# Performance work log

Measured on AMD Instinct MI355X. Metric: run time of the kernel, lower is better.

Reference implementation:

```python
import math
import jax, jax.numpy as jnp
from jax import lax
import numpy as np

HIDDEN = 128
KQ_CH = HIDDEN * 3  # 384
H, W = 48, 64
N = 4


def _conv(x, w, pad, dil):
    # NCHW conv, OIHW weights, stride 1
    return lax.conv_general_dilated(
        x, w, window_strides=(1, 1),
        padding=[(pad, pad), (pad, pad)],
        rhs_dilation=(dil, dil),
        dimension_numbers=("NCHW", "OIHW", "NCHW"))


def _lrelu(x):
    return jnp.where(x >= 0, x, 0.2 * x)


def setup_inputs() -> dict:
    key = jax.random.key(0)
    ks = jax.random.split(key, 7)
    s = 0.05
    return {
        "k": jax.random.normal(ks[0], (N, KQ_CH, H, W), jnp.float32),
        "q": jax.random.normal(ks[1], (N, KQ_CH, H, W), jnp.float32),
        "v": jax.random.normal(ks[2], (N, HIDDEN, H, W), jnp.float32),
        "w_value": jax.random.normal(ks[3], (HIDDEN, HIDDEN, 1, 1), jnp.float32) * s,
        "w_out": jax.random.normal(ks[4], (HIDDEN, HIDDEN, 3, 3), jnp.float32) * s,
        "w_ff1": jax.random.normal(ks[5], (HIDDEN, HIDDEN, 3, 3), jnp.float32) * s,
        "w_ff2": jax.random.normal(ks[6], (HIDDEN, HIDDEN, 3, 3), jnp.float32) * s,
    }


def reference(k, q, v, w_value, w_out, w_ff1, w_ff2):
    n, c, h, w = k.shape  # c = kq_channels
    hw = h * w
    # value embedding: 1x1 conv
    val = _conv(v, w_value, 0, 1)  # [n, hidden, h, w]
    kf = k.reshape(n, c, hw)
    qf = q.reshape(n, c, hw)
    # scores[n, key_pos, query_pos] = k^T q / sqrt(c)
    scores = jnp.einsum("nck,ncq->nkq", kf, qf) / math.sqrt(c)
    # softmax over key positions (torch dim=-2)
    p_attn = jax.nn.softmax(scores, axis=1)  # [n, hw, hw]
    # p_val = value @ p_attn
    p_val = jnp.einsum("ndk,nkq->ndq", val.reshape(n, -1, hw), p_attn)
    p_val = p_val.reshape(v.shape)
    # residual update with output_linear (conv3x3 + LeakyReLU)
    v2 = v + _lrelu(_conv(p_val, w_out, 1, 1))
    # dilated-conv feed forward with residual
    ff = _lrelu(_conv(_lrelu(_conv(v2, w_ff1, 2, 2)), w_ff2, 1, 1))
    return v2 + ff
```

## Files before the change

kernel.cpp:

```cpp
#include <hip/hip_runtime.h>

#define NB  4
#define CKQ 384
#define DH  128
#define HH  48
#define WW  64
#define HW  3072

#define NSPLIT 16
#define KSEG  (HW / NSPLIT)
#define BQ 128
#define BK 32
#define VSP 40
#define PTS 40

typedef short bf16x8 __attribute__((ext_vector_type(8)));
typedef short b16x4  __attribute__((ext_vector_type(4)));
typedef float f32x4  __attribute__((ext_vector_type(4)));
typedef long  i64;
typedef long  i64x2 __attribute__((ext_vector_type(2)));
typedef unsigned short u16;
typedef unsigned int   u32;
typedef unsigned char  u8;
typedef unsigned long long u64;

__device__ __forceinline__ float b2f(u16 u){
  union { u32 i; float f; } x; x.i = ((u32)u) << 16; return x.f;
}
__device__ __forceinline__ u16 f2b(float f){
  union { float f; u32 i; } x; x.f = f;
  u32 r = (x.i + 0x7fffu + ((x.i >> 16) & 1u)) >> 16;
  return (u16)r;
}
__device__ __forceinline__ u8 f2f8(float f){
  return (u8)(__builtin_amdgcn_cvt_pk_fp8_f32(f, f, 0, false) & 0xff);
}

__global__ __launch_bounds__(256)
void tcast8(const float* __restrict__ kin, const float* __restrict__ qin,
            u8* __restrict__ kt8, u8* __restrict__ qt8){
  __shared__ u8 T[64][40];
  const int zz = blockIdx.z;
  const float* in = (zz < NB) ? kin : qin;
  u8* out         = (zz < NB) ? kt8 : qt8;
  const int n  = zz & (NB - 1);
  const int c0 = blockIdx.y * 32;
  const int p0 = blockIdx.x * 64;
  const int tx = threadIdx.x & 63;
  const int ty = threadIdx.x >> 6;
  const float* ib = in + ((size_t)n * CKQ + c0) * HW + p0;
  #pragma unroll
  for (int r = 0; r < 32; r += 4){
    float f = ib[(size_t)(r + ty) * HW + tx];
    T[tx][r + ty] = f2f8(f);
  }
  __syncthreads();
  const int row = threadIdx.x >> 2;
  const int g   = threadIdx.x & 3;
  *(u64*)(out + ((size_t)n * HW + p0 + row) * CKQ + c0 + g * 8)
      = *(const u64*)&T[row][g * 8];
}

__global__ __launch_bounds__(256)
void wprep3(const float* __restrict__ w0, const float* __restrict__ w1,
            const float* __restrict__ w2, u16* __restrict__ o0,
            u16* __restrict__ o1, u16* __restrict__ o2){
  const float* w = (blockIdx.y == 0) ? w0 : (blockIdx.y == 1) ? w1 : w2;
  u16* wt        = (blockIdx.y == 0) ? o0 : (blockIdx.y == 1) ? o1 : o2;
  int idx = blockIdx.x * 256 + threadIdx.x;
  int d = idx >> 7, c = idx & 127;
  #pragma unroll
  for (int tap = 0; tap < 9; ++tap)
    wt[((size_t)tap * DH + d) * DH + c] = f2b(w[(size_t)idx * 9 + tap]);
}

__global__ __launch_bounds__(256)
void val_embed8(const float* __restrict__ v, const float* __restrict__ wv,
                u8* __restrict__ val8){
  int p  = blockIdx.x * 256 + threadIdx.x;
  int d0 = blockIdx.y * 4;
  int n  = blockIdx.z;
  const float* vb = v + (size_t)n * DH * HW;
  float a0 = 0.f, a1 = 0.f, a2 = 0.f, a3 = 0.f;
  for (int c = 0; c < DH; ++c){
    float vv = vb[c * HW + p];
    a0 += wv[(d0 + 0) * DH + c] * vv;
    a1 += wv[(d0 + 1) * DH + c] * vv;
    a2 += wv[(d0 + 2) * DH + c] * vv;
    a3 += wv[(d0 + 3) * DH + c] * vv;
  }
  u8* ob = val8 + (size_t)n * DH * HW;
  ob[(d0 + 0) * HW + p] = f2f8(a0);
  ob[(d0 + 1) * HW + p] = f2f8(a1);
  ob[(d0 + 2) * HW + p] = f2f8(a2);
  ob[(d0 + 3) * HW + p] = f2f8(a3);
}

__global__ __launch_bounds__(256, 3)
void attn8(const u8* __restrict__ kt, const u8* __restrict__ qt,
           const u8* __restrict__ val, u16* __restrict__ outp,
           float* __restrict__ lsum){
  __shared__ u8 Ks[BK * CKQ];
  __shared__ u8 Vs[DH * VSP];
  __shared__ u8 Pt[BQ * PTS];

  const int tid  = threadIdx.x;
  const int wv   = tid >> 6;
  const int lane = tid & 63;
  const int quad = lane >> 4;
  const int l15  = lane & 15;
  const int n    = blockIdx.z;
  const int seg  = blockIdx.y;
  const int j0   = blockIdx.x * BQ;
  const int jra  = wv * 32 + l15;
  const int jrb  = jra + 16;
  const int ja   = j0 + jra;
  const int jb   = j0 + jrb;

  const u8* qrowa = qt + ((size_t)n * HW + ja) * CKQ;
  const u8* qrowb = qt + ((size_t)n * HW + jb) * CKQ;
  i64 qfa[12], qfb[12];
  #pragma unroll
  for (int cs = 0; cs < 12; ++cs){
    qfa[cs] = *(const i64*)&qrowa[cs * 32 + quad * 8];
    qfb[cs] = *(const i64*)&qrowb[cs * 32 + quad * 8];
  }

  const f32x4 zero = {0.f, 0.f, 0.f, 0.f};
  f32x4 oa[8], obacc[8];
  #pragma unroll
  for (int i = 0; i < 8; ++i){ oa[i] = zero; obacc[i] = zero; }
  float la = 0.f, lbv = 0.f;

  const u8* ktb = kt  + (size_t)n * CKQ * HW;
  const u8* vb  = val + (size_t)n * DH * HW;
  const float scale = 0.05103103630798287f;

  for (int it = 0; it < KSEG / BK; ++it){
    const int i0 = seg * KSEG + it * BK;
    for (int idx = tid; idx < BK * 24; idx += 256){
      int i  = idx / 24;
      int g2 = idx % 24;
      i64x2 dv = *(const i64x2*)&ktb[(size_t)(i0 + i) * CKQ + g2 * 16];
      int g0 = 2 * g2, g1 = g0 + 1;
      int gs0 = (g0 & ~7) | ((g0 ^ i) & 7);
      int gs1 = (g1 & ~7) | ((g1 ^ i) & 7);
      *(i64*)&Ks[i * CKQ + gs0 * 8] = dv[0];
      *(i64*)&Ks[i * CKQ + gs1 * 8] = dv[1];
    }
    for (int idx = tid; idx < DH * 4; idx += 256){
      int dd = idx >> 2;
      int c8 = idx & 3;
      *(i64*)&Vs[dd * VSP + c8 * 8] = *(const i64*)&vb[(size_t)dd * HW + i0 + c8 * 8];
    }
    __syncthreads();

    f32x4 s0a = zero, s1a = zero, s0b = zero, s1b = zero;
    #pragma unroll
    for (int cs = 0; cs < 12; ++cs){
      int g  = 4 * cs + quad;
      int gs = (g & ~7) | ((g ^ l15) & 7);
      i64 a0 = *(const i64*)&Ks[l15 * CKQ + gs * 8];
      i64 a1 = *(const i64*)&Ks[(16 + l15) * CKQ + gs * 8];
      s0a = __builtin_amdgcn_mfma_f32_16x16x32_fp8_fp8(a0, qfa[cs], s0a, 0, 0, 0);
      s1a = __builtin_amdgcn_mfma_f32_16x16x32_fp8_fp8(a1, qfa[cs], s1a, 0, 0, 0);
      s0b = __builtin_amdgcn_mfma_f32_16x16x32_fp8_fp8(a0, qfb[cs], s0b, 0, 0, 0);
      s1b = __builtin_amdgcn_mfma_f32_16x16x32_fp8_fp8(a1, qfb[cs], s1b, 0, 0, 0);
    }

    float pa[8], pb[8]; float tsa = 0.f, tsb = 0.f;
    #pragma unroll
    for (int r = 0; r < 4; ++r){
      pa[r]     = __expf(s0a[r] * scale);
      pa[4 + r] = __expf(s1a[r] * scale);
      pb[r]     = __expf(s0b[r] * scale);
      pb[4 + r] = __expf(s1b[r] * scale);
    }
    #pragma unroll
    for (int i = 0; i < 8; ++i){ tsa += pa[i]; tsb += pb[i]; }
    la += tsa; lbv += tsb;

    u32 wa0 = __builtin_amdgcn_cvt_pk_fp8_f32(pa[0], pa[1], 0, false);
    wa0     = __builtin_amdgcn_cvt_pk_fp8_f32(pa[2], pa[3], wa0, true);
    u32 wa1 = __builtin_amdgcn_cvt_pk_fp8_f32(pa[4], pa[5], 0, false);
    wa1     = __builtin_amdgcn_cvt_pk_fp8_f32(pa[6], pa[7], wa1, true);
    u32 wb0 = __builtin_amdgcn_cvt_pk_fp8_f32(pb[0], pb[1], 0, false);
    wb0     = __builtin_amdgcn_cvt_pk_fp8_f32(pb[2], pb[3], wb0, true);
    u32 wb1 = __builtin_amdgcn_cvt_pk_fp8_f32(pb[4], pb[5], 0, false);
    wb1     = __builtin_amdgcn_cvt_pk_fp8_f32(pb[6], pb[7], wb1, true);
    *(u32*)&Pt[jra * PTS + quad * 4]      = wa0;
    *(u32*)&Pt[jra * PTS + 16 + quad * 4] = wa1;
    *(u32*)&Pt[jrb * PTS + quad * 4]      = wb0;
    *(u32*)&Pt[jrb * PTS + 16 + quad * 4] = wb1;
    __builtin_amdgcn_wave_barrier();

    i64 bpa = *(const i64*)&Pt[jra * PTS + quad * 8];
    i64 bpb = *(const i64*)&Pt[jrb * PTS + quad * 8];
    #pragma unroll
    for (int dt = 0; dt < 8; ++dt){
      i64 av = *(const i64*)&Vs[(dt * 16 + l15) * VSP + quad * 8];
      oa[dt]    = __builtin_amdgcn_mfma_f32_16x16x32_fp8_fp8(av, bpa, oa[dt], 0, 0, 0);
      obacc[dt] = __builtin_amdgcn_mfma_f32_16x16x32_fp8_fp8(av, bpb, obacc[dt], 0, 0, 0);
    }
    __syncthreads();
  }

  la  += __shfl_xor(la, 16);  la  += __shfl_xor(la, 32);
  lbv += __shfl_xor(lbv, 16); lbv += __shfl_xor(lbv, 32);

  u16* obp = outp + ((size_t)(seg * NB + n) * HW) * DH;
  #pragma unroll
  for (int dt = 0; dt < 8; ++dt){
    b16x4 pka = { (short)f2b(oa[dt][0]), (short)f2b(oa[dt][1]),
                  (short)f2b(oa[dt][2]), (short)f2b(oa[dt][3]) };
    b16x4 pkb = { (short)f2b(obacc[dt][0]), (short)f2b(obacc[dt][1]),
                  (short)f2b(obacc[dt][2]), (short)f2b(obacc[dt][3]) };
    *(b16x4*)&obp[(size_t)ja * DH + dt * 16 + quad * 4] = pka;
    *(b16x4*)&obp[(size_t)jb * DH + dt * 16 + quad * 4] = pkb;
  }
  if (quad == 0){
    lsum[(size_t)(seg * NB + n) * HW + ja] = la;
    lsum[(size_t)(seg * NB + n) * HW + jb] = lbv;
  }
}

__global__ __launch_bounds__(256)
void combine(const u16* __restrict__ ob, const float* __restrict__ lb,
             u16* __restrict__ pval_t){
  size_t flat = (size_t)blockIdx.x * 256 + threadIdx.x;
  int d = (int)(flat & 127);
  size_t nj = flat >> 7;
  int j = (int)(nj % HW);
  int n = (int)(nj / HW);
  float acc = 0.f, ls = 0.f;
  #pragma unroll
  for (int s = 0; s < NSPLIT; ++s){
    acc += b2f(ob[((size_t)(s * NB + n) * HW + j) * DH + d]);
    ls  += lb[(size_t)(s * NB + n) * HW + j];
  }
  pval_t[flat] = f2b(acc / ls);
}

template<int DIL, int RESM, int OUTM>
__global__ __launch_bounds__(256, 3)
void mconv(const u16* __restrict__ in_t, const u16* __restrict__ wt,
           const void* __restrict__ res, void* __restrict__ out){
  const int tid  = threadIdx.x;
  const int w    = tid >> 6;
  const int lane = tid & 63;
  const int quad = lane >> 4;
  const int l15  = lane & 15;
  const int n    = blockIdx.z;
  const int p0   = blockIdx.x * 32;
  const int d0   = (blockIdx.y * 4 + w) * 16;
  const int y    = p0 >> 6;
  const int x0   = p0 & 63;

  const u16* ib = in_t + (size_t)n * HW * DH;
  f32x4 acc0 = {0.f, 0.f, 0.f, 0.f};
  f32x4 acc1 = {0.f, 0.f, 0.f, 0.f};
  const bf16x8 bzero = {0, 0, 0, 0, 0, 0, 0, 0};

  #pragma unroll
  for (int tap = 0; tap < 9; ++tap){
    const int dy = (tap / 3 - 1) * DIL;
    const int dx = (tap % 3 - 1) * DIL;
    if ((unsigned)(y + dy) >= (unsigned)HH) continue;
    const int off = dy * WW + dx;
    const bool vx0 = (unsigned)(x0 + l15 + dx)      < (unsigned)WW;
    const bool vx1 = (unsigned)(x0 + 16 + l15 + dx) < (unsigned)WW;
    const u16* brow0 = ib + (size_t)(p0 + l15 + off) * DH;
    const u16* brow1 = brow0 + (size_t)16 * DH;
    const u16* wrow  = wt + ((size_t)tap * DH + d0 + l15) * DH;
    #pragma unroll
    for (int c0 = 0; c0 < DH; c0 += 32){
      bf16x8 af = *(const bf16x8*)&wrow[c0 + quad * 8];
      bf16x8 b0 = bzero, b1 = bzero;
      if (vx0) b0 = *(const bf16x8*)&brow0[c0 + quad * 8];
      if (vx1) b1 = *(const bf16x8*)&brow1[c0 + quad * 8];
      acc0 = __builtin_amdgcn_mfma_f32_16x16x32_bf16(af, b0, acc0, 0, 0, 0);
      acc1 = __builtin_amdgcn_mfma_f32_16x16x32_bf16(af, b1, acc1, 0, 0, 0);
    }
  }

  #pragma unroll
  for (int pt = 0; pt < 2; ++pt){
    f32x4 a = pt ? acc1 : acc0;
    const int p = p0 + pt * 16 + l15;
    float v4[4];
    #pragma unroll
    for (int r = 0; r < 4; ++r){
      float vv = a[r];
      vv = (vv >= 0.f) ? vv : 0.2f * vv;
      if (RESM == 1)
        vv += ((const float*)res)[((size_t)n * DH + d0 + quad * 4 + r) * HW + p];
      v4[r] = vv;
    }
    if (RESM == 2){
      b16x4 rv = *(const b16x4*)&((const u16*)res)[((size_t)n * HW + p) * DH + d0 + quad * 4];
      #pragma unroll
      for (int r = 0; r < 4; ++r) v4[r] += b2f((u16)rv[r]);
    }
    if (OUTM == 0){
      b16x4 pk = { (short)f2b(v4[0]), (short)f2b(v4[1]),
                   (short)f2b(v4[2]), (short)f2b(v4[3]) };
      *(b16x4*)&((u16*)out)[((size_t)n * HW + p) * DH + d0 + quad * 4] = pk;
    } else {
      #pragma unroll
      for (int r = 0; r < 4; ++r)
        ((float*)out)[((size_t)n * DH + d0 + quad * 4 + r) * HW + p] = v4[r];
    }
  }
}

extern "C" void kernel_launch(void* const* d_in, const int* in_sizes, int n_in,
                              void* d_out, int out_size, void* d_ws, size_t ws_size,
                              hipStream_t stream){
  const float* k    = (const float*)d_in[0];
  const float* q    = (const float*)d_in[1];
  const float* v    = (const float*)d_in[2];
  const float* wv   = (const float*)d_in[3];
  const float* wout = (const float*)d_in[4];
  const float* wff1 = (const float*)d_in[5];
  const float* wff2 = (const float*)d_in[6];
  float* out = (float*)d_out;

  const size_t TEN  = (size_t)NB * DH * HW;
  const size_t KTEN = (size_t)NB * CKQ * HW;
  const size_t WT   = (size_t)9 * DH * DH;
  u8*  kt8    = (u8*)d_ws;
  u8*  qt8    = kt8 + KTEN;
  u8*  val8   = qt8 + KTEN;
  u16* wt1    = (u16*)(val8 + TEN);
  u16* wt2    = wt1 + WT;
  u16* wt3    = wt2 + WT;
  u16* pval_t = wt3 + WT;
  u16* v2_t   = pval_t + TEN;
  u16* tmid_t = v2_t + TEN;
  u16* ob     = tmid_t + TEN;
  float* lb   = (float*)(ob + (size_t)NSPLIT * TEN);

  tcast8    <<<dim3(48, 12, 2 * NB), 256, 0, stream>>>(k, q, kt8, qt8);
  wprep3    <<<dim3(64, 3), 256, 0, stream>>>(wout, wff1, wff2, wt1, wt2, wt3);
  val_embed8<<<dim3(12, 32, NB), 256, 0, stream>>>(v, wv, val8);
  attn8     <<<dim3(HW / BQ, NSPLIT, NB), 256, 0, stream>>>(kt8, qt8, val8, ob, lb);
  combine   <<<dim3((unsigned)(TEN / 256)), 256, 0, stream>>>(ob, lb, pval_t);
  mconv<1, 1, 0><<<dim3(96, 2, NB), 256, 0, stream>>>(pval_t, wt1, (const void*)v,    (void*)v2_t);
  mconv<2, 0, 0><<<dim3(96, 2, NB), 256, 0, stream>>>(v2_t,   wt2, (const void*)nullptr, (void*)tmid_t);
  mconv<1, 2, 1><<<dim3(96, 2, NB), 256, 0, stream>>>(tmid_t, wt3, (const void*)v2_t, (void*)out);
}
```

Before: 287.7 us.

## Prefetch K/V tiles into registers, halve key splits, widen transpose-cast blocks

The attention kernel now loads the next K and V tiles from global memory into registers while the current tile's MFMA work runs, which hides load latency behind compute. NSPLIT drops from 16 to 8, so there are fewer partial outputs to write and combine, but also fewer blocks and a longer serial loop per block. The k/q fp8 transpose-cast kernel now handles all 384 channels per block with a larger shared tile, giving fully contiguous row stores. The trade-offs are more register pressure from the prefetch buffers and lower parallelism in the attention grid.

Result: slower. 299.9 us (+4.2%).

```diff
diff --git a/kernel.cpp b/kernel.cpp
--- a/kernel.cpp
+++ b/kernel.cpp
@@ -7,10 +7,11 @@
 #define WW  64
 #define HW  3072
 
-#define NSPLIT 16
+#define NSPLIT 8
 #define KSEG  (HW / NSPLIT)
 #define BQ 128
 #define BK 32
+#define NIT (KSEG / BK)
 #define VSP 40
 #define PTS 40
 
@@ -39,26 +40,27 @@
 __global__ __launch_bounds__(256)
 void tcast8(const float* __restrict__ kin, const float* __restrict__ qin,
             u8* __restrict__ kt8, u8* __restrict__ qt8){
-  __shared__ u8 T[64][40];
-  const int zz = blockIdx.z;
-  const float* in = (zz < NB) ? kin : qin;
-  u8* out         = (zz < NB) ? kt8 : qt8;
-  const int n  = zz & (NB - 1);
-  const int c0 = blockIdx.y * 32;
+  __shared__ u8 T[64][392];
+  const int yy = blockIdx.y;
+  const float* in = (yy < NB) ? kin : qin;
+  u8* out         = (yy < NB) ? kt8 : qt8;
+  const int n  = yy & (NB - 1);
   const int p0 = blockIdx.x * 64;
   const int tx = threadIdx.x & 63;
   const int ty = threadIdx.x >> 6;
-  const float* ib = in + ((size_t)n * CKQ + c0) * HW + p0;
-  #pragma unroll
-  for (int r = 0; r < 32; r += 4){
-    float f = ib[(size_t)(r + ty) * HW + tx];
-    T[tx][r + ty] = f2f8(f);
-  }
+  const float* ib = in + (size_t)n * CKQ * HW + p0;
+  #pragma unroll 4
+  for (int c = ty; c < CKQ; c += 4)
+    T[tx][c] = f2f8(ib[(size_t)c * HW + tx]);
   __syncthreads();
-  const int row = threadIdx.x >> 2;
-  const int g   = threadIdx.x & 3;
-  *(u64*)(out + ((size_t)n * HW + p0 + row) * CKQ + c0 + g * 8)
-      = *(const u64*)&T[row][g * 8];
+  u8* ob = out + ((size_t)n * HW + p0) * CKQ;
+  #pragma unroll
+  for (int it = 0; it < 12; ++it){
+    int ch  = it * 256 + threadIdx.x;
+    int row = ch / 48;
+    int g   = ch - row * 48;
+    *(u64*)(ob + (size_t)row * CKQ + g * 8) = *(const u64*)&T[row][g * 8];
+  }
 }
 
 __global__ __launch_bounds__(256)
@@ -117,6 +119,12 @@
   const int ja   = j0 + jra;
   const int jb   = j0 + jrb;
 
+  const u8* ktb = kt  + (size_t)n * CKQ * HW;
+  const u8* vb  = val + (size_t)n * DH * HW;
+
+  const int ki[3] = { tid, tid + 256, tid + 512 };
+  const int vi0 = tid, vi1 = tid + 256;
+
   const u8* qrowa = qt + ((size_t)n * HW + ja) * CKQ;
   const u8* qrowb = qt + ((size_t)n * HW + jb) * CKQ;
   i64 qfa[12], qfb[12];
@@ -132,28 +140,44 @@
   for (int i = 0; i < 8; ++i){ oa[i] = zero; obacc[i] = zero; }
   float la = 0.f, lbv = 0.f;
 
-  const u8* ktb = kt  + (size_t)n * CKQ * HW;
-  const u8* vb  = val + (size_t)n * DH * HW;
   const float scale = 0.05103103630798287f;
 
-  for (int it = 0; it < KSEG / BK; ++it){
-    const int i0 = seg * KSEG + it * BK;
-    for (int idx = tid; idx < BK * 24; idx += 256){
-      int i  = idx / 24;
-      int g2 = idx % 24;
-      i64x2 dv = *(const i64x2*)&ktb[(size_t)(i0 + i) * CKQ + g2 * 16];
+  i64x2 kr[3]; i64 vr[2];
+  {
+    const int i0 = seg * KSEG;
+    #pragma unroll
+    for (int r = 0; r < 3; ++r){
+      int i = ki[r] / 24, g2 = ki[r] % 24;
+      kr[r] = *(const i64x2*)&ktb[(size_t)(i0 + i) * CKQ + g2 * 16];
+    }
+    vr[0] = *(const i64*)&vb[(size_t)(vi0 >> 2) * HW + i0 + (vi0 & 3) * 8];
+    vr[1] = *(const i64*)&vb[(size_t)(vi1 >> 2) * HW + i0 + (vi1 & 3) * 8];
+  }
+
+  for (int it = 0; it < NIT; ++it){
+    #pragma unroll
+    for (int r = 0; r < 3; ++r){
+      int i = ki[r] / 24, g2 = ki[r] % 24;
       int g0 = 2 * g2, g1 = g0 + 1;
       int gs0 = (g0 & ~7) | ((g0 ^ i) & 7);
       int gs1 = (g1 & ~7) | ((g1 ^ i) & 7);
-      *(i64*)&Ks[i * CKQ + gs0 * 8] = dv[0];
-      *(i64*)&Ks[i * CKQ + gs1 * 8] = dv[1];
-    }
-    for (int idx = tid; idx < DH * 4; idx += 256){
-      int dd = idx >> 2;
-      int c8 = idx & 3;
-      *(i64*)&Vs[dd * VSP + c8 * 8] = *(const i64*)&vb[(size_t)dd * HW + i0 + c8 * 8];
-    }
+      *(i64*)&Ks[i * CKQ + gs0 * 8] = kr[r][0];
+      *(i64*)&Ks[i * CKQ + gs1 * 8] = kr[r][1];
+    }
+    *(i64*)&Vs[(vi0 >> 2) * VSP + (vi0 & 3) * 8] = vr[0];
+    *(i64*)&Vs[(vi1 >> 2) * VSP + (vi1 & 3) * 8] = vr[1];
     __syncthreads();
+
+    if (it + 1 < NIT){
+      const int i0n = seg * KSEG + (it + 1) * BK;
+      #pragma unroll
+      for (int r = 0; r < 3; ++r){
+        int i = ki[r] / 24, g2 = ki[r] % 24;
+        kr[r] = *(const i64x2*)&ktb[(size_t)(i0n + i) * CKQ + g2 * 16];
+      }
+      vr[0] = *(const i64*)&vb[(size_t)(vi0 >> 2) * HW + i0n + (vi0 & 3) * 8];
+      vr[1] = *(const i64*)&vb[(size_t)(vi1 >> 2) * HW + i0n + (vi1 & 3) * 8];
+    }
 
     f32x4 s0a = zero, s1a = zero, s0b = zero, s1b = zero;
     #pragma unroll
@@ -340,7 +364,7 @@
   u16* ob     = tmid_t + TEN;
   float* lb   = (float*)(ob + (size_t)NSPLIT * TEN);
 
-  tcast8    <<<dim3(48, 12, 2 * NB), 256, 0, stream>>>(k, q, kt8, qt8);
+  tcast8    <<<dim3(48, 2 * NB), 256, 0, stream>>>(k, q, kt8, qt8);
   wprep3    <<<dim3(64, 3), 256, 0, stream>>>(wout, wff1, wff2, wt1, wt2, wt3);
   val_embed8<<<dim3(12, 32, NB), 256, 0, stream>>>(v, wv, val8);
   attn8     <<<dim3(HW / BQ, NSPLIT, NB), 256, 0, stream>>>(kt8, qt8, val8, ob, lb);
```

## Stage conv input rows in LDS and pre-swizzle weights into MFMA fragment order

Applied to the files above, without the earlier changes.

The 3x3 conv kernel now loads three full input rows (all 128 channels) into shared memory per block and reads the B operands from LDS instead of doing repeated global loads for each tap. The weights are pre-packed into per-lane MFMA fragment order so A loads are contiguous, and the grid is remapped to one image row by 32 output channels per block. The k/q fp8 transpose kernel also now handles all 384 channels per block with wider stores. The trade-off is a larger LDS footprint (about 52KB per block), which may limit occupancy, and each row is staged redundantly by four blocks.

New measurement: 231.9 us. 19.4% less time.

```diff
diff --git a/kernel.cpp b/kernel.cpp
--- a/kernel.cpp
+++ b/kernel.cpp
@@ -13,6 +13,7 @@
 #define BK 32
 #define VSP 40
 #define PTS 40
+#define XROW 136
 
 typedef short bf16x8 __attribute__((ext_vector_type(8)));
 typedef short b16x4  __attribute__((ext_vector_type(4)));
@@ -39,26 +40,27 @@
 __global__ __launch_bounds__(256)
 void tcast8(const float* __restrict__ kin, const float* __restrict__ qin,
             u8* __restrict__ kt8, u8* __restrict__ qt8){
-  __shared__ u8 T[64][40];
-  const int zz = blockIdx.z;
-  const float* in = (zz < NB) ? kin : qin;
-  u8* out         = (zz < NB) ? kt8 : qt8;
-  const int n  = zz & (NB - 1);
-  const int c0 = blockIdx.y * 32;
+  __shared__ u8 T[64][392];
+  const int yy = blockIdx.y;
+  const float* in = (yy < NB) ? kin : qin;
+  u8* out         = (yy < NB) ? kt8 : qt8;
+  const int n  = yy & (NB - 1);
   const int p0 = blockIdx.x * 64;
   const int tx = threadIdx.x & 63;
   const int ty = threadIdx.x >> 6;
-  const float* ib = in + ((size_t)n * CKQ + c0) * HW + p0;
-  #pragma unroll
-  for (int r = 0; r < 32; r += 4){
-    float f = ib[(size_t)(r + ty) * HW + tx];
-    T[tx][r + ty] = f2f8(f);
-  }
+  const float* ib = in + (size_t)n * CKQ * HW + p0;
+  #pragma unroll 4
+  for (int c = ty; c < CKQ; c += 4)
+    T[tx][c] = f2f8(ib[(size_t)c * HW + tx]);
   __syncthreads();
-  const int row = threadIdx.x >> 2;
-  const int g   = threadIdx.x & 3;
-  *(u64*)(out + ((size_t)n * HW + p0 + row) * CKQ + c0 + g * 8)
-      = *(const u64*)&T[row][g * 8];
+  u8* ob = out + ((size_t)n * HW + p0) * CKQ;
+  #pragma unroll
+  for (int it = 0; it < 12; ++it){
+    int ch  = it * 256 + threadIdx.x;
+    int row = ch / 48;
+    int g   = ch - row * 48;
+    *(u64*)(ob + (size_t)row * CKQ + g * 8) = *(const u64*)&T[row][g * 8];
+  }
 }
 
 __global__ __launch_bounds__(256)
@@ -67,11 +69,20 @@
             u16* __restrict__ o1, u16* __restrict__ o2){
   const float* w = (blockIdx.y == 0) ? w0 : (blockIdx.y == 1) ? w1 : w2;
   u16* wt        = (blockIdx.y == 0) ? o0 : (blockIdx.y == 1) ? o1 : o2;
-  int idx = blockIdx.x * 256 + threadIdx.x;
-  int d = idx >> 7, c = idx & 127;
-  #pragma unroll
-  for (int tap = 0; tap < 9; ++tap)
-    wt[((size_t)tap * DH + d) * DH + c] = f2b(w[(size_t)idx * 9 + tap]);
+  int g    = blockIdx.x * 256 + threadIdx.x;
+  int fid  = g >> 6;
+  int lane = g & 63;
+  int l15  = lane & 15, quad = lane >> 4;
+  int tap  = fid >> 5;
+  int cst  = (fid >> 3) & 3;
+  int dt   = fid & 7;
+  int d    = dt * 16 + l15;
+  u16* dst = wt + (size_t)fid * 512 + lane * 8;
+  #pragma unroll
+  for (int e = 0; e < 8; ++e){
+    int c = cst * 32 + quad * 8 + e;
+    dst[e] = f2b(w[((size_t)d * DH + c) * 9 + tap]);
+  }
 }
 
 __global__ __launch_bounds__(256)
@@ -243,72 +254,89 @@
 
 template<int DIL, int RESM, int OUTM>
 __global__ __launch_bounds__(256, 3)
-void mconv(const u16* __restrict__ in_t, const u16* __restrict__ wt,
+void mconv(const u16* __restrict__ in_t, const u16* __restrict__ wtf,
            const void* __restrict__ res, void* __restrict__ out){
+  __shared__ u16 Xs[3 * 64 * XROW];
+
   const int tid  = threadIdx.x;
   const int w    = tid >> 6;
   const int lane = tid & 63;
   const int quad = lane >> 4;
   const int l15  = lane & 15;
   const int n    = blockIdx.z;
-  const int p0   = blockIdx.x * 32;
-  const int d0   = (blockIdx.y * 4 + w) * 16;
-  const int y    = p0 >> 6;
-  const int x0   = p0 & 63;
-
-  const u16* ib = in_t + (size_t)n * HW * DH;
-  f32x4 acc0 = {0.f, 0.f, 0.f, 0.f};
-  f32x4 acc1 = {0.f, 0.f, 0.f, 0.f};
-  const bf16x8 bzero = {0, 0, 0, 0, 0, 0, 0, 0};
+  const int y    = blockIdx.x;
+  const int by   = blockIdx.y;
+  const int xw   = w * 16;
+
+  const bf16x8 bz8 = {0,0,0,0,0,0,0,0};
+  #pragma unroll
+  for (int yi = 0; yi < 3; ++yi){
+    int ysrc = y + (yi - 1) * DIL;
+    bool ok = (unsigned)ysrc < (unsigned)HH;
+    #pragma unroll
+    for (int pass = 0; pass < 4; ++pass){
+      int ch = pass * 256 + tid;
+      int x  = ch >> 4;
+      int g  = ch & 15;
+      bf16x8 v = bz8;
+      if (ok)
+        v = *(const bf16x8*)&in_t[((size_t)n * HW + ysrc * WW + x) * DH + g * 8];
+      *(bf16x8*)&Xs[(yi * 64 + x) * XROW + g * 8] = v;
+    }
+  }
+  __syncthreads();
+
+  f32x4 acc[2];
+  acc[0] = (f32x4){0.f, 0.f, 0.f, 0.f};
+  acc[1] = (f32x4){0.f, 0.f, 0.f, 0.f};
 
   #pragma unroll
   for (int tap = 0; tap < 9; ++tap){
-    const int dy = (tap / 3 - 1) * DIL;
+    const int yi = tap / 3;
     const int dx = (tap % 3 - 1) * DIL;
-    if ((unsigned)(y + dy) >= (unsigned)HH) continue;
-    const int off = dy * WW + dx;
-    const bool vx0 = (unsigned)(x0 + l15 + dx)      < (unsigned)WW;
-    const bool vx1 = (unsigned)(x0 + 16 + l15 + dx) < (unsigned)WW;
-    const u16* brow0 = ib + (size_t)(p0 + l15 + off) * DH;
-    const u16* brow1 = brow0 + (size_t)16 * DH;
-    const u16* wrow  = wt + ((size_t)tap * DH + d0 + l15) * DH;
-    #pragma unroll
-    for (int c0 = 0; c0 < DH; c0 += 32){
-      bf16x8 af = *(const bf16x8*)&wrow[c0 + quad * 8];
-      bf16x8 b0 = bzero, b1 = bzero;
-      if (vx0) b0 = *(const bf16x8*)&brow0[c0 + quad * 8];
-      if (vx1) b1 = *(const bf16x8*)&brow1[c0 + quad * 8];
-      acc0 = __builtin_amdgcn_mfma_f32_16x16x32_bf16(af, b0, acc0, 0, 0, 0);
-      acc1 = __builtin_amdgcn_mfma_f32_16x16x32_bf16(af, b1, acc1, 0, 0, 0);
-    }
-  }
-
-  #pragma unroll
-  for (int pt = 0; pt < 2; ++pt){
-    f32x4 a = pt ? acc1 : acc0;
-    const int p = p0 + pt * 16 + l15;
+    const int xp = xw + l15 + dx;
+    const bool vx = (unsigned)xp < (unsigned)WW;
+    const int xc = vx ? xp : 0;
+    const u16* xrow = &Xs[(yi * 64 + xc) * XROW];
+    #pragma unroll
+    for (int cst = 0; cst < 4; ++cst){
+      bf16x8 bf = bz8;
+      if (vx) bf = *(const bf16x8*)&xrow[cst * 32 + quad * 8];
+      #pragma unroll
+      for (int dt = 0; dt < 2; ++dt){
+        int fid = (tap * 4 + cst) * 8 + by * 2 + dt;
+        bf16x8 af = *(const bf16x8*)&wtf[(size_t)fid * 512 + lane * 8];
+        acc[dt] = __builtin_amdgcn_mfma_f32_16x16x32_bf16(af, bf, acc[dt], 0, 0, 0);
+      }
+    }
+  }
+
+  const int p = y * WW + xw + l15;
+  #pragma unroll
+  for (int dt = 0; dt < 2; ++dt){
+    const int d0q = by * 32 + dt * 16 + quad * 4;
     float v4[4];
     #pragma unroll
     for (int r = 0; r < 4; ++r){
-      float vv = a[r];
+      float vv = acc[dt][r];
       vv = (vv >= 0.f) ? vv : 0.2f * vv;
       if (RESM == 1)
-        vv += ((const float*)res)[((size_t)n * DH + d0 + quad * 4 + r) * HW + p];
+        vv += ((const float*)res)[((size_t)n * DH + d0q + r) * HW + p];
       v4[r] = vv;
     }
     if (RESM == 2){
-      b16x4 rv = *(const b16x4*)&((const u16*)res)[((size_t)n * HW + p) * DH + d0 + quad * 4];
+      b16x4 rv = *(const b16x4*)&((const u16*)res)[((size_t)n * HW + p) * DH + d0q];
       #pragma unroll
       for (int r = 0; r < 4; ++r) v4[r] += b2f((u16)rv[r]);
     }
     if (OUTM == 0){
       b16x4 pk = { (short)f2b(v4[0]), (short)f2b(v4[1]),
                    (short)f2b(v4[2]), (short)f2b(v4[3]) };
-      *(b16x4*)&((u16*)out)[((size_t)n * HW + p) * DH + d0 + quad * 4] = pk;
+      *(b16x4*)&((u16*)out)[((size_t)n * HW + p) * DH + d0q] = pk;
     } else {
       #pragma unroll
       for (int r = 0; r < 4; ++r)
-        ((float*)out)[((size_t)n * DH + d0 + quad * 4 + r) * HW + p] = v4[r];
+        ((float*)out)[((size_t)n * DH + d0q + r) * HW + p] = v4[r];
     }
   }
 }
@@ -340,12 +368,12 @@
   u16* ob     = tmid_t + TEN;
   float* lb   = (float*)(ob + (size_t)NSPLIT * TEN);
 
-  tcast8    <<<dim3(48, 12, 2 * NB), 256, 0, stream>>>(k, q, kt8, qt8);
-  wprep3    <<<dim3(64, 3), 256, 0, stream>>>(wout, wff1, wff2, wt1, wt2, wt3);
+  tcast8    <<<dim3(48, 2 * NB), 256, 0, stream>>>(k, q, kt8, qt8);
+  wprep3    <<<dim3(72, 3), 256, 0, stream>>>(wout, wff1, wff2, wt1, wt2, wt3);
   val_embed8<<<dim3(12, 32, NB), 256, 0, stream>>>(v, wv, val8);
   attn8     <<<dim3(HW / BQ, NSPLIT, NB), 256, 0, stream>>>(kt8, qt8, val8, ob, lb);
   combine   <<<dim3((unsigned)(TEN / 256)), 256, 0, stream>>>(ob, lb, pval_t);
-  mconv<1, 1, 0><<<dim3(96, 2, NB), 256, 0, stream>>>(pval_t, wt1, (const void*)v,    (void*)v2_t);
-  mconv<2, 0, 0><<<dim3(96, 2, NB), 256, 0, stream>>>(v2_t,   wt2, (const void*)nullptr, (void*)tmid_t);
-  mconv<1, 2, 1><<<dim3(96, 2, NB), 256, 0, stream>>>(tmid_t, wt3, (const void*)v2_t, (void*)out);
-}
+  mconv<1, 1, 0><<<dim3(48, 4, NB), 256, 0, stream>>>(pval_t, wt1, (const void*)v,    (void*)v2_t);
+  mconv<2, 0, 0><<<dim3(48, 4, NB), 256, 0, stream>>>(v2_t,   wt2, (const void*)nullptr, (void*)tmid_t);
+  mconv<1, 2, 1><<<dim3(48, 4, NB), 256, 0, stream>>>(tmid_t, wt3, (const void*)v2_t, (void*)out);
+}
```
